# Performance work log

Hardware: AMD Instinct MI355X
Metric: run time of the kernel (lower is better)

## Reference

```python
import jax, jax.numpy as jnp
import numpy as np

BN_EPS = 1e-5


def _gin(x, src, dst, w1, b1, w2, b2):
    # GINConv with eps=0: h_i = MLP(x_i + sum_{j->i} x_j)
    n = x.shape[0]
    agg = jax.ops.segment_sum(x[src], dst, num_segments=n)  # [N, d]
    h = x + agg
    h = jnp.maximum(h @ w1 + b1, 0.0)
    return h @ w2 + b2


def _bn(h, g, beta):
    # BatchNorm1d, training mode (batch stats over nodes, biased var)
    m = h.mean(axis=0)
    v = h.var(axis=0)
    return (h - m) * jax.lax.rsqrt(v + BN_EPS) * g + beta


def setup_inputs() -> dict:
    key = jax.random.key(0)
    ks = jax.random.split(key, 12)
    N, E, D_IN, H, D_OUT = 100000, 1600000, 128, 128, 3
    s = lambda fan_in: 1.0 / np.sqrt(fan_in)
    inp = {
        "x": jax.random.normal(ks[0], (N, D_IN), jnp.float32),
        "edge_index": jax.random.randint(ks[1], (2, E), 0, N, jnp.int32),
        "head_w1": jax.random.normal(ks[2], (D_IN, 256), jnp.float32) * s(D_IN),
        "head_b1": jnp.zeros((256,), jnp.float32),
        "head_w2": jax.random.normal(ks[3], (256, H), jnp.float32) * s(256),
        "head_b2": jnp.zeros((H,), jnp.float32),
        "head_g": jnp.ones((H,), jnp.float32),
        "head_beta": jnp.zeros((H,), jnp.float32),
        "res_w1": jax.random.normal(ks[4], (6, H, H), jnp.float32) * s(H),
        "res_b1": jnp.zeros((6, H), jnp.float32),
        "res_w2": jax.random.normal(ks[5], (6, H, H), jnp.float32) * s(H),
        "res_b2": jnp.zeros((6, H), jnp.float32),
        "res_g": jnp.ones((6, H), jnp.float32),
        "res_beta": jnp.zeros((6, H), jnp.float32),
        "tail_w1": jax.random.normal(ks[6], (H, 32), jnp.float32) * s(H),
        "tail_b1": jnp.zeros((32,), jnp.float32),
        "tail_w2": jax.random.normal(ks[7], (32, D_OUT), jnp.float32) * s(32),
        "tail_b2": jnp.zeros((D_OUT,), jnp.float32),
    }
    return inp


def reference(x, edge_index, head_w1, head_b1, head_w2, head_b2, head_g, head_beta,
              res_w1, res_b1, res_w2, res_b2, res_g, res_beta,
              tail_w1, tail_b1, tail_w2, tail_b2):
    src, dst = edge_index[0], edge_index[1]
    # head: GIN -> BN -> ReLU
    out = _gin(x, src, dst, head_w1, head_b1, head_w2, head_b2)
    out = jnp.maximum(_bn(out, head_g, head_beta), 0.0)
    # 3 residual blocks, each with 2 (GIN -> BN -> ReLU) units
    for blk in range(3):
        identity = out
        for u in (2 * blk, 2 * blk + 1):
            out = _gin(out, src, dst, res_w1[u], res_b1[u], res_w2[u], res_b2[u])
            out = jnp.maximum(_bn(out, res_g[u], res_beta[u]), 0.0)
        out = out + identity
    # tail: GIN only (relu_bn=False)
    out = _gin(out, src, dst, tail_w1, tail_b1, tail_w2, tail_b2)
    return out
```

## Files before the change

### kernel.cpp

```cpp
#include <hip/hip_runtime.h>
#include <cstdint>

#define HDIM 128
#define BN_EPS_F 1e-5f
#define BSHIFT 6

typedef _Float16 half8 __attribute__((ext_vector_type(8)));
typedef _Float16 half4v __attribute__((ext_vector_type(4)));
typedef _Float16 half2v __attribute__((ext_vector_type(2)));
typedef float f32x4 __attribute__((ext_vector_type(4)));

#define PA 136
#define PW 72

__global__ __launch_bounds__(256) void bucket_hist(const int* __restrict__ dst, int E,
                                                   int* __restrict__ bcnt, int NBUK) {
  __shared__ int lcnt[2048];
  int tid = threadIdx.x;
  for (int k = tid; k < 2048; k += 256) lcnt[k] = 0;
  __syncthreads();
  int i = blockIdx.x * blockDim.x + tid;
  int stride = gridDim.x * blockDim.x;
  for (; i < E; i += stride) atomicAdd(&lcnt[dst[i] >> BSHIFT], 1);
  __syncthreads();
  for (int k = tid; k < NBUK; k += 256) {
    int v = lcnt[k];
    if (v) atomicAdd(&bcnt[k], v);
  }
}

__global__ __launch_bounds__(1024) void bucket_scan(const int* __restrict__ bcnt,
    int* __restrict__ bbase, int* __restrict__ bcur, int NBUK, int E) {
  __shared__ int sd[1024];
  int t = threadIdx.x;
  int c0 = (2 * t < NBUK) ? bcnt[2 * t] : 0;
  int c1 = (2 * t + 1 < NBUK) ? bcnt[2 * t + 1] : 0;
  sd[t] = c0 + c1;
  __syncthreads();
  for (int o = 1; o < 1024; o <<= 1) {
    int v = (t >= o) ? sd[t - o] : 0;
    __syncthreads();
    sd[t] += v;
    __syncthreads();
  }
  int excl = sd[t] - (c0 + c1);
  if (2 * t < NBUK) { bbase[2 * t] = excl; bcur[2 * t] = excl; }
  if (2 * t + 1 < NBUK) { bbase[2 * t + 1] = excl + c0; bcur[2 * t + 1] = excl + c0; }
  if (t == 0) bbase[NBUK] = E;
}

__global__ __launch_bounds__(256) void bucket_scatter(const int* __restrict__ src,
    const int* __restrict__ dst, int E, int* __restrict__ bcur, int2* __restrict__ pairs) {
  int i = blockIdx.x * blockDim.x + threadIdx.x;
  int stride = gridDim.x * blockDim.x;
  for (; i < E; i += stride) {
    int d = dst[i];
    int p = atomicAdd(&bcur[d >> BSHIFT], 1);
    pairs[p] = make_int2(src[i], d);
  }
}

__global__ __launch_bounds__(256) void csr_build(const int2* __restrict__ pairs,
    const int* __restrict__ bbase, int* __restrict__ rowptr, int* __restrict__ col,
    int N, int NBUK) {
  __shared__ int cnt[64];
  __shared__ int off[65];
  int b = blockIdx.x, tid = threadIdx.x;
  int s = bbase[b], e = bbase[b + 1];
  if (tid < 64) cnt[tid] = 0;
  __syncthreads();
  for (int i = s + tid; i < e; i += 256) atomicAdd(&cnt[pairs[i].y & 63], 1);
  __syncthreads();
  if (tid == 0) {
    int r = 0;
    for (int k = 0; k < 64; ++k) { off[k] = r; r += cnt[k]; }
    off[64] = r;
  }
  __syncthreads();
  int node0 = b << BSHIFT;
  if (tid < 64) {
    int node = node0 + tid;
    if (node < N) rowptr[node] = s + off[tid];
    cnt[tid] = off[tid];
  }
  __syncthreads();
  for (int i = s + tid; i < e; i += 256) {
    int2 p = pairs[i];
    int pos = atomicAdd(&cnt[p.y & 63], 1);
    col[s + pos] = p.x;
  }
  if (b == 0 && tid == 0) rowptr[N] = bbase[NBUK];
}

__global__ __launch_bounds__(256) void wprep_all(const float* __restrict__ hw1,
    const float* __restrict__ hw2, const float* __restrict__ rw1, const float* __restrict__ rw2,
    _Float16* __restrict__ hi, _Float16* __restrict__ lo) {
  int gid = blockIdx.x * 256 + threadIdx.x;
  if (gid >= 262144) return;
  const float* W;
  int K, Nn, off;
  if (gid < 32768) { W = hw1; K = 128; Nn = 256; off = 0; }
  else if (gid < 65536) { W = hw2; K = 256; Nn = 128; off = 32768; }
  else {
    int j = (gid - 65536) >> 14;
    int u = j >> 1;
    W = (j & 1) ? rw2 + (size_t)u * 16384 : rw1 + (size_t)u * 16384;
    K = 128; Nn = 128; off = 65536 + j * 16384;
  }
  int idx = gid - off;
  int n = idx / K, k = idx - n * K;
  float v = W[(size_t)k * Nn + n];
  _Float16 h = (_Float16)v;
  hi[gid] = h;
  lo[gid] = (_Float16)(v - (float)h);
}

__global__ __launch_bounds__(256) void xcvt_kernel(const float* __restrict__ x,
    _Float16* __restrict__ y, int nv4) {
  int i = blockIdx.x * 256 + threadIdx.x;
  int stride = gridDim.x * 256;
  for (; i < nv4; i += stride) {
    float4 v = ((const float4*)x)[i];
    half4v h = {(_Float16)v.x, (_Float16)v.y, (_Float16)v.z, (_Float16)v.w};
    *(half4v*)&y[(size_t)i * 4] = h;
  }
}

template <int BNT>
__global__ __launch_bounds__(256) void agg_f16_kernel(const _Float16* __restrict__ Y,
    float* __restrict__ A, const int* __restrict__ rowptr, const int* __restrict__ col,
    const float* __restrict__ pstats, const float* __restrict__ pg,
    const float* __restrict__ pbeta, float invN, int N) {
  int node = blockIdx.x * 4 + (threadIdx.x >> 6);
  if (node >= N) return;
  int lane = threadIdx.x & 63;
  float a0 = 1.f, a1 = 1.f, b0 = 0.f, b1 = 0.f;
  if constexpr (BNT) {
    int c0 = 2 * lane, c1 = c0 + 1;
    float m0 = pstats[c0] * invN, m1 = pstats[c1] * invN;
    float v0 = fmaxf(pstats[128 + c0] * invN - m0 * m0, 0.f);
    float v1 = fmaxf(pstats[128 + c1] * invN - m1 * m1, 0.f);
    a0 = pg[c0] * rsqrtf(v0 + BN_EPS_F);
    a1 = pg[c1] * rsqrtf(v1 + BN_EPS_F);
    b0 = pbeta[c0] - m0 * a0;
    b1 = pbeta[c1] - m1 * a1;
  }
  const half2v* Yv = (const half2v*)Y;
  size_t rb = (size_t)node * 64 + lane;
  float2 acc;
  {
    half2v h = Yv[rb];
    float wx = (float)h[0], wy = (float)h[1];
    if constexpr (BNT) {
      wx = fmaxf(fmaf(wx, a0, b0), 0.f);
      wy = fmaxf(fmaf(wy, a1, b1), 0.f);
    }
    acc.x = wx; acc.y = wy;
  }
  int s = rowptr[node], e = rowptr[node + 1];
  int i = s;
  for (; i + 8 <= e; i += 8) {
    half2v t[8];
#pragma unroll
    for (int u = 0; u < 8; ++u) t[u] = Yv[(size_t)col[i + u] * 64 + lane];
#pragma unroll
    for (int u = 0; u < 8; ++u) {
      float wx = (float)t[u][0], wy = (float)t[u][1];
      if constexpr (BNT) {
        wx = fmaxf(fmaf(wx, a0, b0), 0.f);
        wy = fmaxf(fmaf(wy, a1, b1), 0.f);
      }
      acc.x += wx; acc.y += wy;
    }
  }
  for (; i < e; ++i) {
    half2v t = Yv[(size_t)col[i] * 64 + lane];
    float wx = (float)t[0], wy = (float)t[1];
    if constexpr (BNT) {
      wx = fmaxf(fmaf(wx, a0, b0), 0.f);
      wy = fmaxf(fmaf(wy, a1, b1), 0.f);
    }
    acc.x += wx; acc.y += wy;
  }
  ((float2*)A)[rb] = acc;
}

__device__ __forceinline__ void stage_w_slab(_Float16* dsth, _Float16* dstl,
    const _Float16* __restrict__ gh, const _Float16* __restrict__ gl, int stride, int koff) {
  int tid = threadIdx.x;
#pragma unroll
  for (int it = 0; it < 4; ++it) {
    int l = tid + it * 256;
    int r = l >> 3, ch = (l & 7) * 8;
    *(half8*)&dsth[r * PW + ch] = *(const half8*)&gh[(size_t)r * stride + koff + ch];
    *(half8*)&dstl[r * PW + ch] = *(const half8*)&gl[(size_t)r * stride + koff + ch];
  }
}

template <int MF>
__device__ __forceinline__ void gemm_slab(const _Float16* Sh, const _Float16* Sl,
    const _Float16* Wh, const _Float16* Wl, int rowbase, int l15, int l4, int wc, int slab,
    f32x4 (&acc)[MF][4]) {
#pragma unroll
  for (int split = 0; split < 3; ++split) {
    const _Float16* as = (split == 1) ? Sl : Sh;
    const _Float16* bs = (split == 2) ? Wl : Wh;
#pragma unroll
    for (int kf = 0; kf < 2; ++kf) {
      int ka = slab * 64 + kf * 32 + l4 * 8;
      int kw = kf * 32 + l4 * 8;
      half8 a[MF], b[4];
#pragma unroll
      for (int m = 0; m < MF; ++m)
        a[m] = *(const half8*)&as[(rowbase + m * 16 + l15) * PA + ka];
#pragma unroll
      for (int f = 0; f < 4; ++f)
        b[f] = *(const half8*)&bs[(wc * 64 + f * 16 + l15) * PW + kw];
#pragma unroll
      for (int m = 0; m < MF; ++m)
#pragma unroll
        for (int f = 0; f < 4; ++f)
          acc[m][f] = __builtin_amdgcn_mfma_f32_16x16x32_f16(a[m], b[f], acc[m][f], 0, 0, 0);
    }
  }
}

template <int MF, int NH>
__global__ __launch_bounds__(256, 2) void mlp_kernel(
    const float* __restrict__ In, _Float16* __restrict__ Out,
    const _Float16* __restrict__ w1hi, const _Float16* __restrict__ w1lo,
    const float* __restrict__ b1,
    const _Float16* __restrict__ w2hi, const _Float16* __restrict__ w2lo,
    const float* __restrict__ b2, float* __restrict__ stats, int N) {
  constexpr int BM = MF * 32;
  __shared__ _Float16 Ab[2][BM * PA];
  __shared__ _Float16 Wb[2][128 * PW];
  __shared__ _Float16 Hb[NH == 2 ? 2 : 1][NH == 2 ? BM * PA : 1];

  const int tid = threadIdx.x;
  const int wave = tid >> 6, lane = tid & 63;
  const int wr = wave >> 1, wc = wave & 1;
  const int l15 = lane & 15, l4 = lane >> 4;
  const int row0 = blockIdx.x * BM;
  const int rowbase = wr * (MF * 16);

#pragma unroll
  for (int it = 0; it < BM / 8; ++it) {
    int l = tid + it * 256;
    int r = l >> 5, c4 = (l & 31) * 4;
    float4 v = make_float4(0.f, 0.f, 0.f, 0.f);
    if (row0 + r < N) v = *(const float4*)&In[(size_t)(row0 + r) * HDIM + c4];
    half4v hh, ll;
    hh.x = (_Float16)v.x; ll.x = (_Float16)(v.x - (float)hh.x);
    hh.y = (_Float16)v.y; ll.y = (_Float16)(v.y - (float)hh.y);
    hh.z = (_Float16)v.z; ll.z = (_Float16)(v.z - (float)hh.z);
    hh.w = (_Float16)v.w; ll.w = (_Float16)(v.w - (float)hh.w);
    *(half4v*)&Ab[0][r * PA + c4] = hh;
    *(half4v*)&Ab[1][r * PA + c4] = ll;
  }

  _Float16 *Hh, *Hl;
  if constexpr (NH == 2) { Hh = Hb[0]; Hl = Hb[1]; }
  else { Hh = Ab[0]; Hl = Ab[1]; }

  f32x4 acc2[MF][4];
#pragma unroll
  for (int f = 0; f < 4; ++f) {
    float bv = b2[wc * 64 + f * 16 + l15];
#pragma unroll
    for (int m = 0; m < MF; ++m) acc2[m][f] = (f32x4){bv, bv, bv, bv};
  }

  for (int h = 0; h < NH; ++h) {
    f32x4 acc1[MF][4];
#pragma unroll
    for (int f = 0; f < 4; ++f) {
      float bv = b1[h * 128 + wc * 64 + f * 16 + l15];
#pragma unroll
      for (int m = 0; m < MF; ++m) acc1[m][f] = (f32x4){bv, bv, bv, bv};
    }
#pragma unroll
    for (int slab = 0; slab < 2; ++slab) {
      __syncthreads();
      stage_w_slab(Wb[0], Wb[1], w1hi + (size_t)h * 128 * 128, w1lo + (size_t)h * 128 * 128,
                   128, slab * 64);
      __syncthreads();
      gemm_slab<MF>(Ab[0], Ab[1], Wb[0], Wb[1], rowbase, l15, l4, wc, slab, acc1);
    }
    __syncthreads();
#pragma unroll
    for (int m = 0; m < MF; ++m)
#pragma unroll
      for (int f = 0; f < 4; ++f)
#pragma unroll
        for (int r = 0; r < 4; ++r) {
          float v = fmaxf(acc1[m][f][r], 0.f);
          _Float16 hh = (_Float16)v;
          int row = rowbase + m * 16 + l4 * 4 + r;
          int ck = wc * 64 + f * 16 + l15;
          Hh[row * PA + ck] = hh;
          Hl[row * PA + ck] = (_Float16)(v - (float)hh);
        }
#pragma unroll
    for (int slab = 0; slab < 2; ++slab) {
      __syncthreads();
      stage_w_slab(Wb[0], Wb[1], w2hi, w2lo, NH * 128, h * 128 + slab * 64);
      __syncthreads();
      gemm_slab<MF>(Hh, Hl, Wb[0], Wb[1], rowbase, l15, l4, wc, slab, acc2);
    }
  }

  __syncthreads();
  float* psum = (float*)&Wb[0][0];
  float* psq = psum + 256;
#pragma unroll
  for (int f = 0; f < 4; ++f) {
    float s = 0.f, q = 0.f;
#pragma unroll
    for (int m = 0; m < MF; ++m)
#pragma unroll
      for (int r = 0; r < 4; ++r) {
        int grow = row0 + rowbase + m * 16 + l4 * 4 + r;
        float v = acc2[m][f][r];
        if (grow < N) {
          Out[(size_t)grow * HDIM + wc * 64 + f * 16 + l15] = (_Float16)v;
          s += v;
          q += v * v;
        }
      }
    s += __shfl_xor(s, 16); q += __shfl_xor(q, 16);
    s += __shfl_xor(s, 32); q += __shfl_xor(q, 32);
    if (l4 == 0) {
      psum[wr * 128 + wc * 64 + f * 16 + l15] = s;
      psq[wr * 128 + wc * 64 + f * 16 + l15] = q;
    }
  }
  __syncthreads();
  if (tid < 128) {
    atomicAdd(&stats[tid], psum[tid] + psum[128 + tid]);
    atomicAdd(&stats[128 + tid], psq[tid] + psq[128 + tid]);
  }
}

template <int DUAL>
__global__ __launch_bounds__(256) void bnrelu_kernel(
    const _Float16* __restrict__ h1, const float* __restrict__ s1,
    const float* __restrict__ g1, const float* __restrict__ bt1,
    const _Float16* __restrict__ h2, const float* __restrict__ s2,
    const float* __restrict__ g2, const float* __restrict__ bt2,
    _Float16* __restrict__ out, float invN, int nv8) {
  int tid = blockIdx.x * 256 + threadIdx.x;
  int c8 = (tid & 15) * 8;
  float a1[8], r1[8], a2[8], r2[8];
#pragma unroll
  for (int j = 0; j < 8; ++j) {
    int c = c8 + j;
    float m = s1[c] * invN;
    float v = fmaxf(s1[128 + c] * invN - m * m, 0.f);
    a1[j] = g1[c] * rsqrtf(v + BN_EPS_F);
    r1[j] = bt1[c] - m * a1[j];
    if constexpr (DUAL) {
      float m2 = s2[c] * invN;
      float v2 = fmaxf(s2[128 + c] * invN - m2 * m2, 0.f);
      a2[j] = g2[c] * rsqrtf(v2 + BN_EPS_F);
      r2[j] = bt2[c] - m2 * a2[j];
    } else {
      a2[j] = 0.f; r2[j] = 0.f;
    }
  }
  int stride = gridDim.x * 256;
  for (int i = tid; i < nv8; i += stride) {
    half8 u = ((const half8*)h1)[i];
    half8 v = ((const half8*)h2)[i];
    half8 o;
#pragma unroll
    for (int j = 0; j < 8; ++j) {
      float y = fmaxf(fmaf((float)u[j], a1[j], r1[j]), 0.f);
      if constexpr (DUAL) y += fmaxf(fmaf((float)v[j], a2[j], r2[j]), 0.f);
      else y += (float)v[j];
      o[j] = (_Float16)y;
    }
    ((half8*)out)[i] = o;
  }
}

__global__ __launch_bounds__(256, 1) void tail_kernel(
    const float* __restrict__ A, const float* __restrict__ W1, const float* __restrict__ b1,
    const float* __restrict__ W2, const float* __restrict__ b2, float* __restrict__ out, int N) {
  __shared__ float Xs[64][132];
  __shared__ float W1s[128][32];
  __shared__ float H1s[64][36];
  __shared__ float W2s[96];
  __shared__ float b1s[32];
  __shared__ float b2s[3];
  int tid = threadIdx.x;
  int row0 = blockIdx.x * 64;
#pragma unroll
  for (int it = 0; it < 8; ++it) {
    int l = tid + it * 256, r = l >> 5, c4 = l & 31;
    float4 v = make_float4(0.f, 0.f, 0.f, 0.f);
    if (row0 + r < N) v = *(const float4*)&A[(size_t)(row0 + r) * HDIM + c4 * 4];
    *(float4*)&Xs[r][c4 * 4] = v;
  }
#pragma unroll
  for (int it = 0; it < 4; ++it) {
    int l = tid + it * 256;
    int r = l >> 3, c4 = l & 7;
    *(float4*)&W1s[r][c4 * 4] = *(const float4*)&W1[r * 32 + c4 * 4];
  }
  if (tid < 96) W2s[tid] = W2[tid];
  if (tid < 32) b1s[tid] = b1[tid];
  if (tid < 3) b2s[tid] = b2[tid];
  __syncthreads();
  {
    int r = tid >> 2;
    int c0 = (tid & 3) * 8;
    float acc1[8];
#pragma unroll
    for (int j = 0; j < 8; ++j) acc1[j] = b1s[c0 + j];
#pragma unroll 2
    for (int k = 0; k < 128; ++k) {
      float xv = Xs[r][k];
      float4 wA = *(const float4*)&W1s[k][c0];
      float4 wB = *(const float4*)&W1s[k][c0 + 4];
      acc1[0] = fmaf(xv, wA.x, acc1[0]);
      acc1[1] = fmaf(xv, wA.y, acc1[1]);
      acc1[2] = fmaf(xv, wA.z, acc1[2]);
      acc1[3] = fmaf(xv, wA.w, acc1[3]);
      acc1[4] = fmaf(xv, wB.x, acc1[4]);
      acc1[5] = fmaf(xv, wB.y, acc1[5]);
      acc1[6] = fmaf(xv, wB.z, acc1[6]);
      acc1[7] = fmaf(xv, wB.w, acc1[7]);
    }
#pragma unroll
    for (int j = 0; j < 8; ++j) H1s[r][c0 + j] = fmaxf(acc1[j], 0.f);
  }
  __syncthreads();
  if (tid < 192) {
    int r = tid / 3, c = tid - (tid / 3) * 3;
    float accv = b2s[c];
#pragma unroll
    for (int k = 0; k < 32; ++k) accv = fmaf(H1s[r][k], W2s[k * 3 + c], accv);
    if (row0 + r < N) out[(size_t)(row0 + r) * 3 + c] = accv;
  }
}

extern "C" void kernel_launch(void* const* d_in, const int* in_sizes, int n_in,
                              void* d_out, int out_size, void* d_ws, size_t ws_size,
                              hipStream_t stream) {
  const float* x = (const float*)d_in[0];
  const int* ei = (const int*)d_in[1];
  const float* head_w1 = (const float*)d_in[2];
  const float* head_b1 = (const float*)d_in[3];
  const float* head_w2 = (const float*)d_in[4];
  const float* head_b2 = (const float*)d_in[5];
  const float* head_g = (const float*)d_in[6];
  const float* head_bt = (const float*)d_in[7];
  const float* res_w1 = (const float*)d_in[8];
  const float* res_b1 = (const float*)d_in[9];
  const float* res_w2 = (const float*)d_in[10];
  const float* res_b2 = (const float*)d_in[11];
  const float* res_g = (const float*)d_in[12];
  const float* res_bt = (const float*)d_in[13];
  const float* tail_w1 = (const float*)d_in[14];
  const float* tail_b1 = (const float*)d_in[15];
  const float* tail_w2 = (const float*)d_in[16];
  const float* tail_b2 = (const float*)d_in[17];

  const int N = in_sizes[0] / HDIM;
  const int E = in_sizes[1] / 2;
  const int NBUK = (N + 63) >> BSHIFT;
  const int* srcp = ei;
  const int* dstp = ei + E;

  char* base = (char*)d_ws;
  size_t off = 0;
  auto alloc = [&](size_t bytes) -> void* {
    void* p = base + off;
    off += (bytes + 255) & ~(size_t)255;
    return p;
  };
  _Float16* F0 = (_Float16*)alloc((size_t)N * HDIM * 2);
  _Float16* F1 = (_Float16*)alloc((size_t)N * HDIM * 2);
  _Float16* F2 = (_Float16*)alloc((size_t)N * HDIM * 2);
  _Float16* F3 = (_Float16*)alloc((size_t)N * HDIM * 2);
  float* A = (float*)alloc((size_t)N * HDIM * 4);
  int* colb = (int*)alloc((size_t)E * 4);
  int* rowptr = (int*)alloc((size_t)(N + 1) * 4);
  int* bcnt = (int*)alloc((size_t)NBUK * 4);
  int* bbase = (int*)alloc((size_t)(NBUK + 1) * 4);
  int* bcur = (int*)alloc((size_t)NBUK * 4);
  float* S = (float*)alloc(8 * 256 * 4);
  _Float16* whi = (_Float16*)alloc(262144 * 2);
  _Float16* wlo = (_Float16*)alloc(262144 * 2);
  int2* pairs = (int2*)A;
  _Float16* X16 = F3;
  (void)ws_size; (void)n_in; (void)out_size;

  const float invN = 1.0f / (float)N;
  const int aggGrid = (N + 3) / 4;
  const int gridH = (N + 31) / 32, gridR = (N + 63) / 64;
  const int nv8 = N * (HDIM / 8);

  wprep_all<<<1024, 256, 0, stream>>>(head_w1, head_w2, res_w1, res_w2, whi, wlo);
  xcvt_kernel<<<2048, 256, 0, stream>>>(x, X16, N * (HDIM / 4));
  hipMemsetAsync(bcnt, 0, (size_t)NBUK * 4, stream);
  hipMemsetAsync(S, 0, 8 * 256 * 4, stream);
  bucket_hist<<<512, 256, 0, stream>>>(dstp, E, bcnt, NBUK);
  bucket_scan<<<1, 1024, 0, stream>>>(bcnt, bbase, bcur, NBUK, E);
  bucket_scatter<<<2048, 256, 0, stream>>>(srcp, dstp, E, bcur, pairs);
  csr_build<<<NBUK, 256, 0, stream>>>(pairs, bbase, rowptr, colb, N, NBUK);

  const _Float16* u1h[6]; const _Float16* u1l[6];
  const _Float16* u2h[6]; const _Float16* u2l[6];
  for (int u = 0; u < 6; ++u) {
    u1h[u] = whi + 65536 + u * 32768; u1l[u] = wlo + 65536 + u * 32768;
    u2h[u] = whi + 65536 + u * 32768 + 16384; u2l[u] = wlo + 65536 + u * 32768 + 16384;
  }

  agg_f16_kernel<0><<<aggGrid, 256, 0, stream>>>(X16, A, rowptr, colb,
      nullptr, nullptr, nullptr, invN, N);
  mlp_kernel<1, 2><<<gridH, 256, 0, stream>>>(A, F0, whi, wlo, head_b1,
      whi + 32768, wlo + 32768, head_b2, S, N);
  agg_f16_kernel<1><<<aggGrid, 256, 0, stream>>>(F0, A, rowptr, colb,
      S, head_g, head_bt, invN, N);
  mlp_kernel<2, 1><<<gridR, 256, 0, stream>>>(A, F1, u1h[0], u1l[0], res_b1,
      u2h[0], u2l[0], res_b2, S + 256, N);
  agg_f16_kernel<1><<<aggGrid, 256, 0, stream>>>(F1, A, rowptr, colb,
      S + 256, res_g, res_bt, invN, N);
  mlp_kernel<2, 1><<<gridR, 256, 0, stream>>>(A, F2, u1h[1], u1l[1], res_b1 + HDIM,
      u2h[1], u2l[1], res_b2 + HDIM, S + 512, N);
  bnrelu_kernel<1><<<2048, 256, 0, stream>>>(F2, S + 512, res_g + HDIM, res_bt + HDIM,
      F0, S, head_g, head_bt, F3, invN, nv8);
  agg_f16_kernel<0><<<aggGrid, 256, 0, stream>>>(F3, A, rowptr, colb,
      nullptr, nullptr, nullptr, invN, N);
  mlp_kernel<2, 1><<<gridR, 256, 0, stream>>>(A, F0, u1h[2], u1l[2], res_b1 + 2 * HDIM,
      u2h[2], u2l[2], res_b2 + 2 * HDIM, S + 768, N);
  agg_f16_kernel<1><<<aggGrid, 256, 0, stream>>>(F0, A, rowptr, colb,
      S + 768, res_g + 2 * HDIM, res_bt + 2 * HDIM, invN, N);
  mlp_kernel<2, 1><<<gridR, 256, 0, stream>>>(A, F1, u1h[3], u1l[3], res_b1 + 3 * HDIM,
      u2h[3], u2l[3], res_b2 + 3 * HDIM, S + 1024, N);
  bnrelu_kernel<0><<<2048, 256, 0, stream>>>(F1, S + 1024, res_g + 3 * HDIM,
      res_bt + 3 * HDIM, F3, nullptr, nullptr, nullptr, F2, invN, nv8);
  agg_f16_kernel<0><<<aggGrid, 256, 0, stream>>>(F2, A, rowptr, colb,
      nullptr, nullptr, nullptr, invN, N);
  mlp_kernel<2, 1><<<gridR, 256, 0, stream>>>(A, F0, u1h[4], u1l[4], res_b1 + 4 * HDIM,
      u2h[4], u2l[4], res_b2 + 4 * HDIM, S + 1280, N);
  agg_f16_kernel<1><<<aggGrid, 256, 0, stream>>>(F0, A, rowptr, colb,
      S + 1280, res_g + 4 * HDIM, res_bt + 4 * HDIM, invN, N);
  mlp_kernel<2, 1><<<gridR, 256, 0, stream>>>(A, F1, u1h[5], u1l[5], res_b1 + 5 * HDIM,
      u2h[5], u2l[5], res_b2 + 5 * HDIM, S + 1536, N);
  bnrelu_kernel<0><<<2048, 256, 0, stream>>>(F1, S + 1536, res_g + 5 * HDIM,
      res_bt + 5 * HDIM, F2, nullptr, nullptr, nullptr, F3, invN, nv8);
  agg_f16_kernel<0><<<aggGrid, 256, 0, stream>>>(F3, A, rowptr, colb,
      nullptr, nullptr, nullptr, invN, N);
  tail_kernel<<<gridR, 256, 0, stream>>>(A, tail_w1, tail_b1, tail_w2, tail_b2,
                                         (float*)d_out, N);
}
```

Before: 1.579 ms.

## Rebuild CSR construction with block-local binning into coarse 256-node regions

Replaces the fine-grained (64-node bucket) global-atomic scatter with a two-level radix-style build. Each block bins a 4096-edge chunk in shared memory, reserves space per coarse region with one global atomic, and writes packed 32-bit (src<<8 | dst_low) entries with coalesced stores. A per-region kernel then does a local counting sort into CSR. This cuts global atomic contention and halves the scatter bytes, but it assumes N fits within 512 coarse regions and that src fits in 24 bits.

```diff
diff --git a/kernel.cpp b/kernel.cpp
--- a/kernel.cpp
+++ b/kernel.cpp
@@ -3,7 +3,9 @@
 
 #define HDIM 128
 #define BN_EPS_F 1e-5f
-#define BSHIFT 6
+#define CSH 8
+#define CMAX 512
+#define CHUNK 4096
 
 typedef _Float16 half8 __attribute__((ext_vector_type(8)));
 typedef _Float16 half4v __attribute__((ext_vector_type(4)));
@@ -13,83 +15,139 @@
 #define PA 136
 #define PW 72
 
-__global__ __launch_bounds__(256) void bucket_hist(const int* __restrict__ dst, int E,
-                                                   int* __restrict__ bcnt, int NBUK) {
-  __shared__ int lcnt[2048];
+
+__global__ __launch_bounds__(256) void coarse_hist(const int* __restrict__ dst, int E,
+                                                   int* __restrict__ gcnt) {
+  __shared__ int l[CMAX];
   int tid = threadIdx.x;
-  for (int k = tid; k < 2048; k += 256) lcnt[k] = 0;
+  for (int k = tid; k < CMAX; k += 256) l[k] = 0;
   __syncthreads();
   int i = blockIdx.x * blockDim.x + tid;
   int stride = gridDim.x * blockDim.x;
-  for (; i < E; i += stride) atomicAdd(&lcnt[dst[i] >> BSHIFT], 1);
-  __syncthreads();
-  for (int k = tid; k < NBUK; k += 256) {
-    int v = lcnt[k];
-    if (v) atomicAdd(&bcnt[k], v);
-  }
-}
-
-__global__ __launch_bounds__(1024) void bucket_scan(const int* __restrict__ bcnt,
-    int* __restrict__ bbase, int* __restrict__ bcur, int NBUK, int E) {
-  __shared__ int sd[1024];
+  for (; i < E; i += stride) atomicAdd(&l[dst[i] >> CSH], 1);
+  __syncthreads();
+  for (int k = tid; k < CMAX; k += 256) {
+    int v = l[k];
+    if (v) atomicAdd(&gcnt[k], v);
+  }
+}
+
+__global__ __launch_bounds__(256) void coarse_scan(const int* __restrict__ gcnt,
+    int* __restrict__ gbase, int* __restrict__ gcur, int E) {
+  __shared__ int sd[256];
   int t = threadIdx.x;
-  int c0 = (2 * t < NBUK) ? bcnt[2 * t] : 0;
-  int c1 = (2 * t + 1 < NBUK) ? bcnt[2 * t + 1] : 0;
+  int c0 = gcnt[2 * t], c1 = gcnt[2 * t + 1];
   sd[t] = c0 + c1;
   __syncthreads();
-  for (int o = 1; o < 1024; o <<= 1) {
+  for (int o = 1; o < 256; o <<= 1) {
     int v = (t >= o) ? sd[t - o] : 0;
     __syncthreads();
     sd[t] += v;
     __syncthreads();
   }
   int excl = sd[t] - (c0 + c1);
-  if (2 * t < NBUK) { bbase[2 * t] = excl; bcur[2 * t] = excl; }
-  if (2 * t + 1 < NBUK) { bbase[2 * t + 1] = excl + c0; bcur[2 * t + 1] = excl + c0; }
-  if (t == 0) bbase[NBUK] = E;
-}
-
-__global__ __launch_bounds__(256) void bucket_scatter(const int* __restrict__ src,
-    const int* __restrict__ dst, int E, int* __restrict__ bcur, int2* __restrict__ pairs) {
-  int i = blockIdx.x * blockDim.x + threadIdx.x;
-  int stride = gridDim.x * blockDim.x;
-  for (; i < E; i += stride) {
-    int d = dst[i];
-    int p = atomicAdd(&bcur[d >> BSHIFT], 1);
-    pairs[p] = make_int2(src[i], d);
-  }
-}
-
-__global__ __launch_bounds__(256) void csr_build(const int2* __restrict__ pairs,
-    const int* __restrict__ bbase, int* __restrict__ rowptr, int* __restrict__ col,
-    int N, int NBUK) {
-  __shared__ int cnt[64];
-  __shared__ int off[65];
-  int b = blockIdx.x, tid = threadIdx.x;
-  int s = bbase[b], e = bbase[b + 1];
-  if (tid < 64) cnt[tid] = 0;
-  __syncthreads();
-  for (int i = s + tid; i < e; i += 256) atomicAdd(&cnt[pairs[i].y & 63], 1);
-  __syncthreads();
-  if (tid == 0) {
-    int r = 0;
-    for (int k = 0; k < 64; ++k) { off[k] = r; r += cnt[k]; }
-    off[64] = r;
-  }
-  __syncthreads();
-  int node0 = b << BSHIFT;
-  if (tid < 64) {
-    int node = node0 + tid;
-    if (node < N) rowptr[node] = s + off[tid];
-    cnt[tid] = off[tid];
-  }
+  gbase[2 * t] = excl; gcur[2 * t] = excl;
+  gbase[2 * t + 1] = excl + c0; gcur[2 * t + 1] = excl + c0;
+  if (t == 0) gbase[CMAX] = E;
+}
+
+__global__ __launch_bounds__(256) void bin_chunk(const int* __restrict__ src,
+    const int* __restrict__ dst, int E, int* __restrict__ gcur,
+    unsigned int* __restrict__ binned) {
+  __shared__ int cnt[CMAX];
+  __shared__ int ofs[CMAX];
+  __shared__ int cur[CMAX];
+  __shared__ int gb[CMAX];
+  __shared__ int sd[256];
+  __shared__ unsigned int data[CHUNK];
+  __shared__ unsigned short keyv[CHUNK];
+  const int tid = threadIdx.x;
+  const int c0e = blockIdx.x * CHUNK;
+  const int n = min(CHUNK, E - c0e);
+
+  int ss[CHUNK / 256], dd[CHUNK / 256];
+#pragma unroll
+  for (int k = 0; k < CHUNK / 256; ++k) {
+    int idx = c0e + k * 256 + tid;
+    if (idx < E) { ss[k] = src[idx]; dd[k] = dst[idx]; }
+    else dd[k] = -1;
+  }
+  for (int k = tid; k < CMAX; k += 256) cnt[k] = 0;
+  __syncthreads();
+#pragma unroll
+  for (int k = 0; k < CHUNK / 256; ++k)
+    if (dd[k] >= 0) atomicAdd(&cnt[dd[k] >> CSH], 1);
+  __syncthreads();
+  {
+    int a = cnt[2 * tid], b = cnt[2 * tid + 1];
+    sd[tid] = a + b;
+    __syncthreads();
+    for (int o = 1; o < 256; o <<= 1) {
+      int v = (tid >= o) ? sd[tid - o] : 0;
+      __syncthreads();
+      sd[tid] += v;
+      __syncthreads();
+    }
+    int excl = sd[tid] - (a + b);
+    ofs[2 * tid] = excl; cur[2 * tid] = excl;
+    ofs[2 * tid + 1] = excl + a; cur[2 * tid + 1] = excl + a;
+  }
+  __syncthreads();
+#pragma unroll
+  for (int k = 0; k < CHUNK / 256; ++k) {
+    if (dd[k] >= 0) {
+      int key = dd[k] >> CSH;
+      int p = atomicAdd(&cur[key], 1);
+      data[p] = ((unsigned int)ss[k] << CSH) | (unsigned int)(dd[k] & ((1 << CSH) - 1));
+      keyv[p] = (unsigned short)key;
+    }
+  }
+  __syncthreads();
+  for (int j = tid; j < CMAX; j += 256) {
+    int c = cnt[j];
+    gb[j] = c ? atomicAdd(&gcur[j], c) : 0;
+  }
+  __syncthreads();
+  for (int i = tid; i < n; i += 256) {
+    int k = keyv[i];
+    binned[gb[k] + (i - ofs[k])] = data[i];
+  }
+}
+
+__global__ __launch_bounds__(256) void region_build(const unsigned int* __restrict__ binned,
+    const int* __restrict__ gbase, int* __restrict__ rowptr, int* __restrict__ col,
+    int N, int E) {
+  __shared__ int cnt[256];
+  __shared__ int off[256];
+  __shared__ int sd[256];
+  const int b = blockIdx.x, tid = threadIdx.x;
+  const int s = gbase[b], e = gbase[b + 1];
+  cnt[tid] = 0;
+  __syncthreads();
+  for (int i = s + tid; i < e; i += 256)
+    atomicAdd(&cnt[binned[i] & 255], 1);
+  __syncthreads();
+  int c = cnt[tid];
+  sd[tid] = c;
+  __syncthreads();
+  for (int o = 1; o < 256; o <<= 1) {
+    int v = (tid >= o) ? sd[tid - o] : 0;
+    __syncthreads();
+    sd[tid] += v;
+    __syncthreads();
+  }
+  off[tid] = sd[tid] - c;
+  __syncthreads();
+  int node = (b << CSH) + tid;
+  if (node < N) rowptr[node] = s + off[tid];
+  cnt[tid] = off[tid];
   __syncthreads();
   for (int i = s + tid; i < e; i += 256) {
-    int2 p = pairs[i];
-    int pos = atomicAdd(&cnt[p.y & 63], 1);
-    col[s + pos] = p.x;
-  }
-  if (b == 0 && tid == 0) rowptr[N] = bbase[NBUK];
+    unsigned int v = binned[i];
+    int p = atomicAdd(&cnt[v & 255], 1);
+    col[s + p] = (int)(v >> CSH);
+  }
+  if (b == 0 && tid == 0) rowptr[N] = E;
 }
 
 __global__ __launch_bounds__(256) void wprep_all(const float* __restrict__ hw1,
@@ -469,7 +527,7 @@
 
   const int N = in_sizes[0] / HDIM;
   const int E = in_sizes[1] / 2;
-  const int NBUK = (N + 63) >> BSHIFT;
+  const int NC = (N + 255) >> CSH;
   const int* srcp = ei;
   const int* dstp = ei + E;
 
@@ -487,13 +545,13 @@
   float* A = (float*)alloc((size_t)N * HDIM * 4);
   int* colb = (int*)alloc((size_t)E * 4);
   int* rowptr = (int*)alloc((size_t)(N + 1) * 4);
-  int* bcnt = (int*)alloc((size_t)NBUK * 4);
-  int* bbase = (int*)alloc((size_t)(NBUK + 1) * 4);
-  int* bcur = (int*)alloc((size_t)NBUK * 4);
+  int* gcnt = (int*)alloc((size_t)CMAX * 4);
+  int* gbase = (int*)alloc((size_t)(CMAX + 1) * 4);
+  int* gcur = (int*)alloc((size_t)CMAX * 4);
   float* S = (float*)alloc(8 * 256 * 4);
   _Float16* whi = (_Float16*)alloc(262144 * 2);
   _Float16* wlo = (_Float16*)alloc(262144 * 2);
-  int2* pairs = (int2*)A;
+  unsigned int* binned = (unsigned int*)A;
   _Float16* X16 = F3;
   (void)ws_size; (void)n_in; (void)out_size;
 
@@ -504,12 +562,12 @@
 
   wprep_all<<<1024, 256, 0, stream>>>(head_w1, head_w2, res_w1, res_w2, whi, wlo);
   xcvt_kernel<<<2048, 256, 0, stream>>>(x, X16, N * (HDIM / 4));
-  hipMemsetAsync(bcnt, 0, (size_t)NBUK * 4, stream);
+  hipMemsetAsync(gcnt, 0, (size_t)CMAX * 4, stream);
   hipMemsetAsync(S, 0, 8 * 256 * 4, stream);
-  bucket_hist<<<512, 256, 0, stream>>>(dstp, E, bcnt, NBUK);
-  bucket_scan<<<1, 1024, 0, stream>>>(bcnt, bbase, bcur, NBUK, E);
-  bucket_scatter<<<2048, 256, 0, stream>>>(srcp, dstp, E, bcur, pairs);
-  csr_build<<<NBUK, 256, 0, stream>>>(pairs, bbase, rowptr, colb, N, NBUK);
+  coarse_hist<<<512, 256, 0, stream>>>(dstp, E, gcnt);
+  coarse_scan<<<1, 256, 0, stream>>>(gcnt, gbase, gcur, E);
+  bin_chunk<<<(E + CHUNK - 1) / CHUNK, 256, 0, stream>>>(srcp, dstp, E, gcur, binned);
+  region_build<<<NC, 256, 0, stream>>>(binned, gbase, rowptr, colb, N, E);
 
   const _Float16* u1h[6]; const _Float16* u1l[6];
   const _Float16* u2h[6]; const _Float16* u2l[6];
```

Result: faster. 1.332 ms (-15.6%).
